# Kernel tuning notes

Hardware: AMD Instinct MI355X
Metric: run time of the kernel (lower is better)

The kernel has to match this reference:

```python
import jax, jax.numpy as jnp
import numpy as np

B_SZ, L_SEQ, D_DATA = 2, 1024, 8
D_CTRL = 256
POLY = 40
N_LAYERS = 2
D_STATE = 16
D_CONV = 4
D_INNER = 1 * D_CTRL          # expand_factor_control = 1
DT_RANK = -(-D_CTRL // 16)    # ceil(d_model/16) = 16
EPS = 1e-5


def setup_inputs() -> dict:
    key = jax.random.key(0)
    ks = jax.random.split(key, 12)
    s = 0.02
    x = jax.random.uniform(ks[0], (B_SZ, L_SEQ, D_DATA), dtype=jnp.float32)
    y = jax.random.uniform(ks[1], (B_SZ, L_SEQ, D_DATA), dtype=jnp.float32)
    return {
        'x': x,
        'y': y,
        # control_proj (note: fed 2*d_data features in structured forward)
        'control_proj_w': jax.random.normal(ks[2], (D_CTRL, 2 * D_DATA)) * s,
        'control_proj_b': jnp.zeros((D_CTRL,), jnp.float32),
        # stacked Mamba layer params (leading dim = n_layers)
        'norm_w': jnp.ones((N_LAYERS, D_CTRL), jnp.float32),
        'in_proj_w': jax.random.normal(ks[3], (N_LAYERS, 2 * D_INNER, D_CTRL)) * s,
        'conv_w': jax.random.normal(ks[4], (N_LAYERS, D_INNER, D_CONV)) * s,
        'conv_b': jnp.zeros((N_LAYERS, D_INNER), jnp.float32),
        'x_proj_w': jax.random.normal(ks[5], (N_LAYERS, DT_RANK + 2 * D_STATE, D_INNER)) * s,
        'dt_proj_w': jax.random.normal(ks[6], (N_LAYERS, D_INNER, DT_RANK)) * s,
        'dt_proj_b': jnp.zeros((N_LAYERS, D_INNER), jnp.float32),
        'A_log': jnp.tile(jnp.log(jnp.arange(1, D_STATE + 1, dtype=jnp.float32))[None, None, :], (N_LAYERS, D_INNER, 1)),
        'D_skip': jnp.ones((N_LAYERS, D_INNER), jnp.float32),
        'out_proj_w': jax.random.normal(ks[7], (N_LAYERS, D_CTRL, D_INNER)) * s,
        # b_net: Linear(d_control, 2*d_data*poly_dim^2)
        'b_net_w': jax.random.normal(ks[8], (2 * D_DATA * POLY * POLY, D_CTRL)) * s,
        'b_net_b': jnp.zeros((2 * D_DATA * POLY * POLY,), jnp.float32),
    }


def _rmsnorm(u, w):
    return u * jax.lax.rsqrt(jnp.mean(u * u, axis=-1, keepdims=True) + EPS) * w


def _causal_conv(u, w, b):
    # u: [B,L,C]; w: [C,K] depthwise causal conv, pad left K-1
    K = w.shape[-1]
    L = u.shape[1]
    up = jnp.pad(u, ((0, 0), (K - 1, 0), (0, 0)))
    acc = jnp.zeros_like(u)
    for k in range(K):  # K=4, fixed small kernel
        acc = acc + up[:, k:k + L, :] * w[:, k]
    return acc + b


def _mamba(u, norm_w, in_proj_w, conv_w, conv_b, x_proj_w, dt_proj_w, dt_proj_b, A_log, D_skip, out_proj_w):
    # mambapy-style stack of residual blocks: u = mixer(rmsnorm(u)) + u
    for i in range(N_LAYERS):
        r = _rmsnorm(u, norm_w[i])
        xz = jnp.einsum('bld,ed->ble', r, in_proj_w[i])          # [B,L,2*di]
        xc, zg = jnp.split(xz, 2, axis=-1)
        xc = jax.nn.silu(_causal_conv(xc, conv_w[i], conv_b[i]))  # [B,L,di]
        dbc = jnp.einsum('bld,ed->ble', xc, x_proj_w[i])          # [B,L,dt_rank+2*ds]
        delta = jax.nn.softplus(jnp.einsum('blr,dr->bld', dbc[..., :DT_RANK], dt_proj_w[i]) + dt_proj_b[i])
        Bm = dbc[..., DT_RANK:DT_RANK + D_STATE]
        Cm = dbc[..., DT_RANK + D_STATE:]
        A = -jnp.exp(A_log[i])                                    # [di,ds]
        dA = jnp.exp(delta[..., None] * A)                        # [B,L,di,ds]
        dBx = delta[..., None] * Bm[:, :, None, :] * xc[..., None]

        def step(h, inp):
            dA_t, dBx_t = inp
            h = dA_t * h + dBx_t
            return h, h

        h0 = jnp.zeros((u.shape[0], D_INNER, D_STATE), u.dtype)
        _, hs = jax.lax.scan(step, h0, (dA.transpose(1, 0, 2, 3), dBx.transpose(1, 0, 2, 3)))
        yv = jnp.einsum('lbds,lbs->bld', hs, Cm.transpose(1, 0, 2)) + D_skip[i] * xc
        yv = yv * jax.nn.silu(zg)
        u = jnp.einsum('bld,ed->ble', yv, out_proj_w[i]) + u
    return u


def _power_mat(z):
    # z ** arange(POLY), built with cumprod (grad-safe at exponent 0)
    ones = jnp.ones(z.shape + (1,), z.dtype)
    reps = jnp.broadcast_to(z[..., None], z.shape + (POLY - 1,))
    return jnp.cumprod(jnp.concatenate([ones, reps], axis=-1), axis=-1)  # [B,L,2d,P]


def reference(x, y, control_proj_w, control_proj_b, norm_w, in_proj_w, conv_w, conv_b,
              x_proj_w, dt_proj_w, dt_proj_b, A_log, D_skip, out_proj_w, b_net_w, b_net_b):
    B, L, d = x.shape
    xdot = y - x
    z = jnp.concatenate([x, xdot], axis=-1)                       # [B,L,2d]
    pm = _power_mat(z)                                            # [B,L,2d,P]
    ctrl_in = jnp.flip(jnp.concatenate([xdot, y], axis=-1), axis=1)
    ctrl_in = ctrl_in @ control_proj_w.T + control_proj_b
    sp = _mamba(ctrl_in, norm_w, in_proj_w, conv_w, conv_b, x_proj_w,
                dt_proj_w, dt_proj_b, A_log, D_skip, out_proj_w)
    state_pred = jnp.flip(sp, axis=1)                             # [B,L,d_ctrl]
    bmat = (state_pred @ b_net_w.T + b_net_b).reshape(B, L, 2 * d, POLY, POLY)
    pow1 = jnp.einsum('bldkj,bldk->bldj', bmat, pm)
    zdot = jnp.einsum('bldj,bldj->bld', pow1, jnp.flip(pm, axis=2))
    return zdot[:, 1:, :], state_pred
```

## Files before the change

### kernel.cpp

```cpp
#include <hip/hip_runtime.h>
#include <hip/hip_bf16.h>

#define B_SZ   2
#define LSEQ   1024
#define DD     8
#define DCTRL  256
#define POLY   40
#define NL     2
#define DSTATE 16
#define DCONV  4
#define DINNER 256
#define DTRANK 16
#define NBL    (B_SZ*LSEQ)
#define NROWS  (2*DD*POLY*POLY)
#define NSLOT  25
#define NCH    32
#define LCH    32

typedef __attribute__((ext_vector_type(8))) short bf16x8;
typedef __attribute__((ext_vector_type(8))) unsigned short us8;
typedef __attribute__((ext_vector_type(4))) unsigned short us4;
typedef __attribute__((ext_vector_type(4))) float f32x4;

__device__ __forceinline__ float sigmoidf_(float x){ return 1.f/(1.f+__expf(-x)); }
__device__ __forceinline__ float softplusf_(float x){ return fmaxf(x,0.f) + log1pf(__expf(-fabsf(x))); }
__device__ __forceinline__ unsigned short f2bf(float f){
  unsigned int u = __float_as_uint(f);
  unsigned int r = (u + 0x7fffu + ((u>>16)&1u)) >> 16;
  return (unsigned short)r;
}

__global__ void k_f2bf(const float* __restrict__ in, unsigned short* __restrict__ out, int n8){
  int i = blockIdx.x*blockDim.x + threadIdx.x;
  if (i>=n8) return;
  const float4* p = (const float4*)(in + (size_t)i*8);
  float4 a = p[0], b = p[1];
  us8 r;
  r[0]=f2bf(a.x); r[1]=f2bf(a.y); r[2]=f2bf(a.z); r[3]=f2bf(a.w);
  r[4]=f2bf(b.x); r[5]=f2bf(b.y); r[6]=f2bf(b.z); r[7]=f2bf(b.w);
  *(us8*)(out + (size_t)i*8) = r;
}

#define IPW_N8 (NL*512*256/8)
#define OPW_N8 (NL*256*256/8)
#define PRE_B0 ((IPW_N8+OPW_N8)/256)
#define PRE_B1 (NL*288*256/256)
#define PRE_B2 (16*NBL/256)
#define PRE_B3 (NBL*256/256)
#define PRE_B4 (NROWS*256/8/256)
__global__ void k_prologue(const float* __restrict__ ipw, const float* __restrict__ opw,
                           const float* __restrict__ dtw, const float* __restrict__ xpw,
                           const float* __restrict__ x,   const float* __restrict__ y,
                           const float* __restrict__ cpw, const float* __restrict__ cpb,
                           const float* __restrict__ bnw,
                           unsigned short* __restrict__ ipwb,
                           unsigned short* __restrict__ wcomb,
                           float* __restrict__ pmt, float* __restrict__ u,
                           unsigned short* __restrict__ Wb){
  int bx = blockIdx.x; int tid = threadIdx.x;
  if (bx < PRE_B0){
    int i = bx*256 + tid;
    const float* src = (i < IPW_N8) ? (ipw + (size_t)i*8) : (opw + (size_t)(i-IPW_N8)*8);
    const float4* p = (const float4*)src;
    float4 a = p[0], b = p[1];
    us8 r;
    r[0]=f2bf(a.x); r[1]=f2bf(a.y); r[2]=f2bf(a.z); r[3]=f2bf(a.w);
    r[4]=f2bf(b.x); r[5]=f2bf(b.y); r[6]=f2bf(b.z); r[7]=f2bf(b.w);
    *(us8*)(ipwb + (size_t)i*8) = r;
  } else if (bx < PRE_B0+PRE_B1){
    int idx = (bx-PRE_B0)*256 + tid;
    int e = idx & 255; int row = (idx>>8) % 288; int l = idx / (288*256);
    float v;
    if (row < 256){
      float s=0.f;
      #pragma unroll
      for (int r=0;r<16;++r) s += dtw[((size_t)l*256+row)*16+r] * xpw[((size_t)l*48+r)*256+e];
      v = s;
    } else {
      v = xpw[((size_t)l*48 + (row-240))*256 + e];
    }
    wcomb[idx] = f2bf(v);
  } else if (bx < PRE_B0+PRE_B1+PRE_B2){
    int idx = (bx-PRE_B0-PRE_B1)*256 + tid;
    int m = idx & (NBL-1); int c = idx >> 11;
    float z;
    if (c < 8) z = x[(size_t)m*8 + c];
    else       z = y[(size_t)m*8 + (c-8)] - x[(size_t)m*8 + (c-8)];
    float p = 1.f;
    #pragma unroll
    for (int j=0;j<POLY;++j){ pmt[((size_t)c*POLY+j)*NBL + m] = p; p*=z; }
  } else if (bx < PRE_B0+PRE_B1+PRE_B2+PRE_B3){
    int idx = (bx-PRE_B0-PRE_B1-PRE_B2)*256 + tid;
    int e = idx & 255; int m = idx >> 8;
    int bb = m >> 10; int lm = m & 1023; int lo = 1023 - lm;
    const float* xp = x + ((size_t)bb*1024+lo)*8;
    const float* yp = y + ((size_t)bb*1024+lo)*8;
    const float* wr = cpw + (size_t)e*16;
    float acc = cpb[e];
    #pragma unroll
    for (int d=0; d<8; ++d) acc += (yp[d]-xp[d])*wr[d];
    #pragma unroll
    for (int d=0; d<8; ++d) acc += yp[d]*wr[8+d];
    u[idx] = acc;
  } else {
    int i = (bx-PRE_B0-PRE_B1-PRE_B2-PRE_B3)*256 + tid;
    const float4* p = (const float4*)(bnw + (size_t)i*8);
    float4 a = p[0], b = p[1];
    us8 r;
    r[0]=f2bf(a.x); r[1]=f2bf(a.y); r[2]=f2bf(a.z); r[3]=f2bf(a.w);
    r[4]=f2bf(b.x); r[5]=f2bf(b.y); r[6]=f2bf(b.z); r[7]=f2bf(b.w);
    *(us8*)(Wb + (size_t)i*8) = r;
  }
}

__global__ void k_rms(const float* __restrict__ u, const float* __restrict__ nw,
                      unsigned short* __restrict__ rb){
  int m = blockIdx.x; int e = threadIdx.x;
  float v = u[(size_t)m*256 + e];
  float ss = v*v;
  #pragma unroll
  for (int off=32; off>0; off>>=1) ss += __shfl_down(ss, off);
  __shared__ float sred[4];
  __shared__ float srstd;
  int wid = e>>6; int lane = e&63;
  if (lane==0) sred[wid]=ss;
  __syncthreads();
  if (e==0){ float t = sred[0]+sred[1]+sred[2]+sred[3]; srstd = rsqrtf(t*(1.f/256.f) + 1e-5f); }
  __syncthreads();
  rb[(size_t)m*256+e] = f2bf(v * srstd * nw[e]);
}

__global__ void __launch_bounds__(256)
gemm_bf(const unsigned short* __restrict__ A, const unsigned short* __restrict__ B,
        int N, int K, const float* __restrict__ bias,
        float* __restrict__ C0, float* __restrict__ C1, int ldc, int mode){
  __shared__ __align__(16) unsigned short Asm[128*40];
  __shared__ __align__(16) unsigned short Bsm[64*40];
  int tid = threadIdx.x;
  int lane = tid & 63;
  int w = tid >> 6; int wr = w >> 1, wc = w & 1;
  int l15 = lane & 15, l4 = lane >> 4;
  int m0 = blockIdx.y*128, n0 = blockIdx.x*64;

  f32x4 acc[4][2];
  #pragma unroll
  for (int i=0;i<4;++i)
    #pragma unroll
    for (int j=0;j<2;++j){ acc[i][j][0]=0.f; acc[i][j][1]=0.f; acc[i][j][2]=0.f; acc[i][j][3]=0.f; }

  int nks = K >> 5;
  for (int ks=0; ks<nks; ++ks){
    int k0 = ks*32;
    #pragma unroll
    for (int g2=0; g2<2; ++g2){
      int g = tid + g2*256; int row = g>>2, c8 = g&3;
      *(us8*)&Asm[row*40 + c8*8] = *(const us8*)(A + (size_t)(m0+row)*K + k0 + c8*8);
    }
    {
      int row = tid>>2, c8 = tid&3; int bn = n0+row;
      us8 v;
      if (bn < N){
        v = *(const us8*)(B + (size_t)bn*K + k0 + c8*8);
      } else {
        for (int z=0;z<8;++z) v[z]=0;
      }
      *(us8*)&Bsm[row*40 + c8*8] = v;
    }
    __syncthreads();
    bf16x8 av[4], bv[2];
    #pragma unroll
    for (int i=0;i<4;++i) av[i] = *(bf16x8*)&Asm[(wr*64+i*16+l15)*40 + l4*8];
    #pragma unroll
    for (int j=0;j<2;++j) bv[j] = *(bf16x8*)&Bsm[(wc*32+j*16+l15)*40 + l4*8];
    #pragma unroll
    for (int i=0;i<4;++i)
      #pragma unroll
      for (int j=0;j<2;++j)
        acc[i][j] = __builtin_amdgcn_mfma_f32_16x16x32_bf16(av[i], bv[j], acc[i][j], 0,0,0);
    __syncthreads();
  }

  #pragma unroll
  for (int i=0;i<4;++i){
    #pragma unroll
    for (int j=0;j<2;++j){
      int n = n0 + wc*32 + j*16 + l15;
      #pragma unroll
      for (int q=0;q<4;++q){
        int m = m0 + wr*64 + i*16 + l4*4 + q;
        float v = acc[i][j][q];
        if (mode==0){
          C0[(size_t)m*ldc + n] = v;
        } else if (mode==1){
          C0[(size_t)m*ldc + n] += v;
        } else {
          if (n < 256) C0[(size_t)m*256 + n] = softplusf_(v + bias[n]);
          else if (n < N) C1[(size_t)m*32 + (n-256)] = v;
        }
      }
    }
  }
}

__global__ void k_convsilu(const float* __restrict__ xz, const float* __restrict__ cw,
                           const float* __restrict__ cb, float* __restrict__ xc,
                           unsigned short* __restrict__ xcb){
  int idx = blockIdx.x*blockDim.x + threadIdx.x;
  if (idx >= NBL*64) return;
  int d4 = (idx & 63) << 2; int m = idx >> 6;
  int bb = m>>10, l = m&1023;
  float4 w0 = *(const float4*)&cw[(d4+0)*4];
  float4 w1 = *(const float4*)&cw[(d4+1)*4];
  float4 w2 = *(const float4*)&cw[(d4+2)*4];
  float4 w3 = *(const float4*)&cw[(d4+3)*4];
  float4 cbv = *(const float4*)&cb[d4];
  float a0=cbv.x, a1=cbv.y, a2=cbv.z, a3=cbv.w;
  #pragma unroll
  for (int k=0;k<4;++k){
    int ls = l - 3 + k;
    if (ls >= 0){
      float4 v = *(const float4*)&xz[((size_t)(bb*1024+ls))*512 + d4];
      a0 += v.x * ((const float*)&w0)[k];
      a1 += v.y * ((const float*)&w1)[k];
      a2 += v.z * ((const float*)&w2)[k];
      a3 += v.w * ((const float*)&w3)[k];
    }
  }
  a0 = a0*sigmoidf_(a0); a1 = a1*sigmoidf_(a1);
  a2 = a2*sigmoidf_(a2); a3 = a3*sigmoidf_(a3);
  float4 o; o.x=a0; o.y=a1; o.z=a2; o.w=a3;
  *(float4*)&xc[(size_t)m*256 + d4] = o;
  us4 ob; ob[0]=f2bf(a0); ob[1]=f2bf(a1); ob[2]=f2bf(a2); ob[3]=f2bf(a3);
  *(us4*)&xcb[(size_t)m*256 + d4] = ob;
}

__global__ void k_scan1(const float* __restrict__ delta, const float* __restrict__ bc,
                        const float* __restrict__ xc, const float* __restrict__ alog,
                        float* __restrict__ hend, float* __restrict__ Pc){
  int blk = blockIdx.x;
  int dg = blk & 15; int ch = (blk>>4) & (NCH-1); int bb = blk >> 9;
  int tid = threadIdx.x; int dl = tid>>4; int s = tid&15; int d = dg*16+dl;
  float A = -__expf(alog[(size_t)d*16+s]);
  float h = 0.f, p = 1.f;
  size_t base = (size_t)bb*1024 + ch*LCH;
  #pragma unroll 4
  for (int t=0;t<LCH;++t){
    size_t mb = base + t;
    float de  = delta[mb*256+d];
    float Bv  = bc[mb*32+s];
    float xcv = xc[mb*256+d];
    float a = __expf(de*A);
    h = a*h + de*Bv*xcv;
    p *= a;
  }
  size_t o = (((size_t)bb*NCH+ch)*256+d)*16+s;
  hend[o]=h; Pc[o]=p;
}

__global__ void k_scan2(const float* __restrict__ hend, const float* __restrict__ Pc,
                        float* __restrict__ Hinit){
  int idx = blockIdx.x*blockDim.x + threadIdx.x;
  if (idx >= B_SZ*256*16) return;
  int bb = idx >> 12; int ds = idx & 4095;
  float H = 0.f;
  #pragma unroll
  for (int ch=0; ch<NCH; ++ch){
    size_t o = ((size_t)bb*NCH+ch)*4096 + ds;
    Hinit[o] = H;
    H = Pc[o]*H + hend[o];
  }
}

__global__ void k_scan3(const float* __restrict__ delta, const float* __restrict__ bc,
                        const float* __restrict__ xc, const float* __restrict__ xz,
                        const float* __restrict__ alog, const float* __restrict__ dskip,
                        const float* __restrict__ Hinit, unsigned short* __restrict__ yvb){
  int blk = blockIdx.x;
  int dg = blk & 15; int ch = (blk>>4) & (NCH-1); int bb = blk >> 9;
  int tid = threadIdx.x; int dl = tid>>4; int s = tid&15; int d = dg*16+dl;
  float A = -__expf(alog[(size_t)d*16+s]);
  float dsk = dskip[d];
  float h = Hinit[(((size_t)bb*NCH+ch)*256+d)*16+s];
  size_t base = (size_t)bb*1024 + ch*LCH;
  #pragma unroll 2
  for (int t=0;t<LCH;++t){
    size_t mb = base + t;
    float de  = delta[mb*256+d];
    float Bv  = bc[mb*32+s];
    float Cv  = bc[mb*32+16+s];
    float xcv = xc[mb*256+d];
    float a = __expf(de*A);
    h = a*h + de*Bv*xcv;
    float yval = h*Cv;
    yval += __shfl_xor(yval,1);
    yval += __shfl_xor(yval,2);
    yval += __shfl_xor(yval,4);
    yval += __shfl_xor(yval,8);
    if (s==0){
      float zg = xz[mb*512+256+d];
      yvb[mb*256+d] = f2bf((yval + dsk*xcv) * zg * sigmoidf_(zg));
    }
  }
}

__global__ void k_storesp(const float* __restrict__ u, float* __restrict__ outsp,
                          unsigned short* __restrict__ spb){
  int idx = blockIdx.x*blockDim.x+threadIdx.x;
  if (idx>=NBL*256) return;
  int e = idx & 255; int m = idx >> 8;
  int bb=m>>10, l=m&1023;
  float v = u[((size_t)(bb*1024 + (1023-l)))*256 + e];
  outsp[idx]=v; spb[idx]=f2bf(v);
}

__global__ void __launch_bounds__(512)
k_bnet_mfma(const unsigned short* __restrict__ spb, const unsigned short* __restrict__ Wb,
            const float* __restrict__ bnb, const float* __restrict__ pmt,
            float* __restrict__ part){
  __shared__ __align__(16) unsigned short Asm[256*40];
  __shared__ __align__(16) unsigned short Bsm[64*40];
  __shared__ float red[2][256];

  int tid = threadIdx.x;
  int lane = tid & 63;
  int w = tid >> 6;
  int wr = w >> 1, wc = w & 1;
  int l15 = lane & 15, l4 = lane >> 4;
  int bx = blockIdx.x;
  int m0 = blockIdx.y*256;
  int n0 = bx*64;

  f32x4 acc[4][2];
  #pragma unroll
  for (int i=0;i<4;++i)
    #pragma unroll
    for (int j=0;j<2;++j){ acc[i][j][0]=0.f; acc[i][j][1]=0.f; acc[i][j][2]=0.f; acc[i][j][3]=0.f; }

  for (int ks=0; ks<8; ++ks){
    int k0 = ks*32;
    #pragma unroll
    for (int g2=0; g2<2; ++g2){
      int g = tid + g2*512;
      int row = g>>2, c8 = g&3;
      *(us8*)&Asm[row*40 + c8*8] = *(const us8*)(spb + ((size_t)(m0+row))*256 + k0 + c8*8);
    }
    if (tid < 256){
      int row = tid>>2, c8 = tid&3;
      *(us8*)&Bsm[row*40 + c8*8] = *(const us8*)(Wb + ((size_t)(n0+row))*256 + k0 + c8*8);
    }
    __syncthreads();
    bf16x8 av[4], bv[2];
    #pragma unroll
    for (int i=0;i<4;++i) av[i] = *(bf16x8*)&Asm[(wr*64+i*16+l15)*40 + l4*8];
    #pragma unroll
    for (int j=0;j<2;++j) bv[j] = *(bf16x8*)&Bsm[(wc*32+j*16+l15)*40 + l4*8];
    #pragma unroll
    for (int i=0;i<4;++i)
      #pragma unroll
      for (int j=0;j<2;++j)
        acc[i][j] = __builtin_amdgcn_mfma_f32_16x16x32_bf16(av[i], bv[j], acc[i][j], 0,0,0);
    __syncthreads();
  }

  int c = bx/25, slot = bx%25;
  int rem0 = slot*64;
  float bnbv[2]; int kkv[2], jjv[2];
  #pragma unroll
  for (int j=0;j<2;++j){
    int nl = wc*32 + j*16 + l15;
    int rem = rem0 + nl;
    bnbv[j] = bnb[n0 + nl];
    kkv[j] = rem/40; jjv[j] = rem%40;
  }
  const float* pc  = pmt + (size_t)c*POLY*NBL;
  const float* pcf = pmt + (size_t)(15-c)*POLY*NBL;
  #pragma unroll
  for (int i=0;i<4;++i){
    int mb = m0 + wr*64 + i*16 + l4*4;
    f32x4 s; s[0]=0.f; s[1]=0.f; s[2]=0.f; s[3]=0.f;
    #pragma unroll
    for (int j=0;j<2;++j){
      f32x4 pk = *(const f32x4*)&pc [(size_t)kkv[j]*NBL + mb];
      f32x4 pj = *(const f32x4*)&pcf[(size_t)jjv[j]*NBL + mb];
      #pragma unroll
      for (int q=0;q<4;++q) s[q] += (acc[i][j][q] + bnbv[j]) * pk[q] * pj[q];
    }
    #pragma unroll
    for (int q=0;q<4;++q){
      float t = s[q];
      t += __shfl_xor(t,1); t += __shfl_xor(t,2);
      t += __shfl_xor(t,4); t += __shfl_xor(t,8);
      if (l15==0) red[wc][wr*64 + i*16 + l4*4 + q] = t;
    }
  }
  __syncthreads();
  if (tid < 256){
    float v = red[0][tid] + red[1][tid];
    part[((size_t)(c*NSLOT + slot))*NBL + m0 + tid] = v;
  }
}

__global__ void k_final(const float* __restrict__ part, float* __restrict__ out){
  int j = blockIdx.x*blockDim.x+threadIdx.x;
  if (j >= 16*2046) return;
  int c = j / 2046; int r = j % 2046;
  int bb = r / 1023; int l = r % 1023 + 1;
  size_t m = (size_t)bb*1024 + l;
  float s = 0.f;
  #pragma unroll
  for (int q=0;q<NSLOT;++q) s += part[((size_t)(c*NSLOT + q))*NBL + m];
  out[((size_t)(bb*1023 + (l-1)))*16 + c] = s;
}

extern "C" void kernel_launch(void* const* d_in, const int* in_sizes, int n_in,
                              void* d_out, int out_size, void* d_ws, size_t ws_size,
                              hipStream_t stream) {
  const float* x    = (const float*)d_in[0];
  const float* y    = (const float*)d_in[1];
  const float* cpw  = (const float*)d_in[2];
  const float* cpb  = (const float*)d_in[3];
  const float* nw   = (const float*)d_in[4];
  const float* ipw  = (const float*)d_in[5];
  const float* cvw  = (const float*)d_in[6];
  const float* cvb  = (const float*)d_in[7];
  const float* xpw  = (const float*)d_in[8];
  const float* dtw  = (const float*)d_in[9];
  const float* dtb  = (const float*)d_in[10];
  const float* alog = (const float*)d_in[11];
  const float* dsk  = (const float*)d_in[12];
  const float* opw  = (const float*)d_in[13];
  const float* bnw  = (const float*)d_in[14];
  const float* bnb  = (const float*)d_in[15];

  float* out      = (float*)d_out;
  float* out_zdot = out;
  float* out_sp   = out + 32736;

  float* ws = (float*)d_ws;
  size_t off = 0;
  float* u     = ws + off; off += (size_t)NBL*256;
  unsigned short* rb = (unsigned short*)(ws + off); off += (size_t)NBL*256/2;
  float* xz    = ws + off; off += (size_t)NBL*512;
  float* xc    = ws + off; off += (size_t)NBL*256;
  unsigned short* xcb = (unsigned short*)(ws + off); off += (size_t)NBL*256/2;
  float* delta = ws + off; off += (size_t)NBL*256;
  float* bcm   = ws + off; off += (size_t)NBL*32;
  unsigned short* yvb = (unsigned short*)(ws + off); off += (size_t)NBL*256/2;
  float* pmt   = ws + off; off += (size_t)NBL*16*POLY;
  float* part  = ws + off; off += (size_t)NSLOT*NBL*16;
  float* hend  = ws + off; off += (size_t)B_SZ*NCH*256*16;
  float* Pc    = ws + off; off += (size_t)B_SZ*NCH*256*16;
  float* Hinit = ws + off; off += (size_t)B_SZ*NCH*256*16;
  unsigned short* spb  = (unsigned short*)(ws + off); off += (size_t)NBL*256/2;
  unsigned short* ipwb = (unsigned short*)(ws + off); off += (size_t)(IPW_N8+OPW_N8);
  unsigned short* wcomb= (unsigned short*)(ws + off); off += (size_t)NL*288*256/2;

  int wbEarly = ((off + (size_t)NROWS*256/2)*sizeof(float) <= ws_size) ? 1 : 0;
  unsigned short* Wb = wbEarly ? (unsigned short*)(ws + off) : (unsigned short*)ws;

  unsigned short* opwb = ipwb + (size_t)IPW_N8*8;

  int preBlocks = PRE_B0+PRE_B1+PRE_B2+PRE_B3 + (wbEarly ? PRE_B4 : 0);
  k_prologue<<<preBlocks, 256, 0, stream>>>(ipw, opw, dtw, xpw, x, y, cpw, cpb, bnw,
                                            ipwb, wcomb, pmt, u, Wb);

  for (int i=0;i<NL;++i){
    k_rms<<<NBL, 256, 0, stream>>>(u, nw + i*256, rb);
    gemm_bf<<<dim3(8,16), 256, 0, stream>>>(rb, ipwb + (size_t)i*512*256, 512, 256,
                                            nullptr, xz, nullptr, 512, 0);
    k_convsilu<<<(NBL*64+255)/256, 256, 0, stream>>>(xz, cvw + i*256*4, cvb + i*256, xc, xcb);
    gemm_bf<<<dim3(5,16), 256, 0, stream>>>(xcb, wcomb + (size_t)i*288*256, 288, 256,
                                            dtb + i*256, delta, bcm, 256, 2);
    k_scan1<<<B_SZ*NCH*16, 256, 0, stream>>>(delta, bcm, xc, alog + (size_t)i*256*16, hend, Pc);
    k_scan2<<<(B_SZ*256*16+255)/256, 256, 0, stream>>>(hend, Pc, Hinit);
    k_scan3<<<B_SZ*NCH*16, 256, 0, stream>>>(delta, bcm, xc, xz, alog + (size_t)i*256*16,
                                             dsk + i*256, Hinit, yvb);
    gemm_bf<<<dim3(4,16), 256, 0, stream>>>(yvb, opwb + (size_t)i*256*256, 256, 256,
                                            nullptr, u, nullptr, 256, 1);
  }

  k_storesp<<<(NBL*256+255)/256, 256, 0, stream>>>(u, out_sp, spb);
  if (!wbEarly){
    k_f2bf<<<(NROWS*256/8 + 255)/256, 256, 0, stream>>>(bnw, Wb, NROWS*256/8);
  }
  k_bnet_mfma<<<dim3(NROWS/64, NBL/256), 512, 0, stream>>>(spb, Wb, bnb, pmt, part);
  k_final<<<(16*2046+255)/256, 256, 0, stream>>>(part, out_zdot);
}
```

Measured before the change: 264.8 us.

## Double-buffer shared-memory tiles in b_net MFMA GEMM with register prefetch

The b_net GEMM kernel now keeps two shared-memory buffers for the A and B tiles. Each thread loads the next K-slice into registers while MFMAs run on the current buffer, then writes it into the other buffer, so only one barrier is needed per iteration instead of two. This is meant to hide global-load latency behind matrix math, at the cost of doubling LDS use and adding register pressure, which may lower occupancy. The workspace offset for ipwb is also enlarged, which looks like a sizing fix that shifts where later buffers sit.

Result: faster. 256.4 us (-3.2%).

```diff
diff --git a/kernel.cpp b/kernel.cpp
--- a/kernel.cpp
+++ b/kernel.cpp
@@ -317,8 +317,8 @@
 k_bnet_mfma(const unsigned short* __restrict__ spb, const unsigned short* __restrict__ Wb,
             const float* __restrict__ bnb, const float* __restrict__ pmt,
             float* __restrict__ part){
-  __shared__ __align__(16) unsigned short Asm[256*40];
-  __shared__ __align__(16) unsigned short Bsm[64*40];
+  __shared__ __align__(16) unsigned short Asm[2][256*40];
+  __shared__ __align__(16) unsigned short Bsm[2][64*40];
   __shared__ float red[2][256];
 
   int tid = threadIdx.x;
@@ -330,36 +330,53 @@
   int m0 = blockIdx.y*256;
   int n0 = bx*64;
 
+  int aRow0 = (tid)>>2,        aC0 = (tid)&3;
+  int aRow1 = (tid+512)>>2,    aC1 = (tid+512)&3;
+  int bRow  = tid>>2,          bC  = tid&3;
+  const unsigned short* aSrc0 = spb + ((size_t)(m0+aRow0))*256 + aC0*8;
+  const unsigned short* aSrc1 = spb + ((size_t)(m0+aRow1))*256 + aC1*8;
+  const unsigned short* bSrc  = Wb  + ((size_t)(n0+bRow ))*256 + bC*8;
+
   f32x4 acc[4][2];
   #pragma unroll
   for (int i=0;i<4;++i)
     #pragma unroll
     for (int j=0;j<2;++j){ acc[i][j][0]=0.f; acc[i][j][1]=0.f; acc[i][j][2]=0.f; acc[i][j][3]=0.f; }
 
+  us8 rA0 = *(const us8*)(aSrc0);
+  us8 rA1 = *(const us8*)(aSrc1);
+  us8 rB;
+  if (tid < 256) rB = *(const us8*)(bSrc);
+  *(us8*)&Asm[0][aRow0*40 + aC0*8] = rA0;
+  *(us8*)&Asm[0][aRow1*40 + aC1*8] = rA1;
+  if (tid < 256) *(us8*)&Bsm[0][bRow*40 + bC*8] = rB;
+  __syncthreads();
+
+  int cur = 0;
   for (int ks=0; ks<8; ++ks){
-    int k0 = ks*32;
-    #pragma unroll
-    for (int g2=0; g2<2; ++g2){
-      int g = tid + g2*512;
-      int row = g>>2, c8 = g&3;
-      *(us8*)&Asm[row*40 + c8*8] = *(const us8*)(spb + ((size_t)(m0+row))*256 + k0 + c8*8);
-    }
-    if (tid < 256){
-      int row = tid>>2, c8 = tid&3;
-      *(us8*)&Bsm[row*40 + c8*8] = *(const us8*)(Wb + ((size_t)(n0+row))*256 + k0 + c8*8);
-    }
-    __syncthreads();
+    if (ks < 7){
+      int k0n = (ks+1)*32;
+      rA0 = *(const us8*)(aSrc0 + k0n);
+      rA1 = *(const us8*)(aSrc1 + k0n);
+      if (tid < 256) rB = *(const us8*)(bSrc + k0n);
+    }
     bf16x8 av[4], bv[2];
     #pragma unroll
-    for (int i=0;i<4;++i) av[i] = *(bf16x8*)&Asm[(wr*64+i*16+l15)*40 + l4*8];
-    #pragma unroll
-    for (int j=0;j<2;++j) bv[j] = *(bf16x8*)&Bsm[(wc*32+j*16+l15)*40 + l4*8];
+    for (int i=0;i<4;++i) av[i] = *(bf16x8*)&Asm[cur][(wr*64+i*16+l15)*40 + l4*8];
+    #pragma unroll
+    for (int j=0;j<2;++j) bv[j] = *(bf16x8*)&Bsm[cur][(wc*32+j*16+l15)*40 + l4*8];
     #pragma unroll
     for (int i=0;i<4;++i)
       #pragma unroll
       for (int j=0;j<2;++j)
         acc[i][j] = __builtin_amdgcn_mfma_f32_16x16x32_bf16(av[i], bv[j], acc[i][j], 0,0,0);
+    if (ks < 7){
+      *(us8*)&Asm[cur^1][aRow0*40 + aC0*8] = rA0;
+      *(us8*)&Asm[cur^1][aRow1*40 + aC1*8] = rA1;
+      if (tid < 256) *(us8*)&Bsm[cur^1][bRow*40 + bC*8] = rB;
+    }
     __syncthreads();
+    cur ^= 1;
   }
 
   int c = bx/25, slot = bx%25;
@@ -452,7 +469,7 @@
   float* Pc    = ws + off; off += (size_t)B_SZ*NCH*256*16;
   float* Hinit = ws + off; off += (size_t)B_SZ*NCH*256*16;
   unsigned short* spb  = (unsigned short*)(ws + off); off += (size_t)NBL*256/2;
-  unsigned short* ipwb = (unsigned short*)(ws + off); off += (size_t)(IPW_N8+OPW_N8);
+  unsigned short* ipwb = (unsigned short*)(ws + off); off += (size_t)(IPW_N8+OPW_N8)*4;
   unsigned short* wcomb= (unsigned short*)(ws + off); off += (size_t)NL*288*256/2;
 
   int wbEarly = ((off + (size_t)NROWS*256/2)*sizeof(float) <= ws_size) ? 1 : 0;
```
